# Kernel tuning notes

Measured on AMD Instinct MI355X. Metric: run time of the kernel, lower is better.

The kernel has to match this reference:

```python
import jax, jax.numpy as jnp
import numpy as np
import math

H = 128  # hidden_dim
RADIUS = 30.0


def _lin(x, w, b):
    return x @ w + b


def _masked_softmax(logits, mask):
    return jax.nn.softmax(jnp.where(mask, logits, -1e9), axis=-1)


def setup_inputs() -> dict:
    key = jax.random.key(0)
    ks = iter(jax.random.split(key, 64))

    def p(shape, s=0.02):
        return (jax.random.normal(next(ks), shape, jnp.float32) * s)

    B, N, T, M, L = 2, 48, 24, 192, 20
    inp = {
        'agents_state': jax.random.normal(next(ks), (B, N, T, 5), jnp.float32),
        'agents_mask': jnp.ones((B, N, T), jnp.float32),
        'map_polylines': jax.random.normal(next(ks), (B, M, L, 2), jnp.float32),
        'map_poly_mask': jnp.ones((B, M), jnp.float32),
        'map_poly_type': jax.random.randint(next(ks), (B, M), 0, 4),
        'map_tl_status': jax.random.randint(next(ks), (B, M), 0, 8),
        'map_on_route': jax.random.randint(next(ks), (B, M), 0, 2),
        # AgentStateEncoder
        'ae_w0': p((5, H)), 'ae_b0': p((H,)), 'ae_w1': p((H, H)), 'ae_b1': p((H,)),
        'ae_w2': p((H, H)), 'ae_b2': p((H,)),
        # MapPolylineNodeEncoder point_mlp
        'mp_w0': p((2, H)), 'mp_b0': p((H,)), 'mp_w1': p((H, H)), 'mp_b1': p((H,)),
        'type_emb': p((4, H)), 'tl_emb': p((8, H)), 'route_emb': p((2, H)),
        'mo_w0': p((H, H)), 'mo_b0': p((H,)), 'mo_w1': p((H, H)), 'mo_b1': p((H,)),
        # map_rel_mlp (3 -> H -> 1)
        'mr_w0': p((3, H)), 'mr_b0': p((H,)), 'mr_w1': p((H, 1)), 'mr_b1': p((1,)),
        # nbr_rel_mlp (5 -> H -> 1)
        'nr_w0': p((5, H)), 'nr_b0': p((H,)), 'nr_w1': p((H, 1)), 'nr_b1': p((1,)),
        # tau_out (3H -> H -> 64)
        'to_w0': p((3 * H, H)), 'to_b0': p((H,)), 'to_w1': p((H, 64)), 'to_b1': p((64,)),
    }
    return inp


def reference(agents_state, agents_mask, map_polylines, map_poly_mask,
              map_poly_type, map_tl_status, map_on_route,
              ae_w0, ae_b0, ae_w1, ae_b1, ae_w2, ae_b2,
              mp_w0, mp_b0, mp_w1, mp_b1, type_emb, tl_emb, route_emb,
              mo_w0, mo_b0, mo_w1, mo_b1,
              mr_w0, mr_b0, mr_w1, mr_b1,
              nr_w0, nr_b0, nr_w1, nr_b1,
              to_w0, to_b0, to_w1, to_b1):
    B, N, T, _ = agents_state.shape
    a_mask = agents_mask > 0.5
    a_feat = agents_state[..., :5]

    # --- MapPolylineNodeEncoder ---
    m = map_poly_mask > 0.5
    h = jax.nn.relu(_lin(jax.nn.relu(_lin(map_polylines, mp_w0, mp_b0)), mp_w1, mp_b1))  # B,M,L,H
    h = h.max(axis=2)  # B,M,H
    pt = jnp.clip(map_poly_type, 0, type_emb.shape[0] - 1)
    tl = jnp.clip(map_tl_status, 0, tl_emb.shape[0] - 1)
    rt = jnp.clip(map_on_route, 0, route_emb.shape[0] - 1)
    h = h + type_emb[pt] + tl_emb[tl] + route_emb[rt]
    h = _lin(jax.nn.relu(_lin(h, mo_w0, mo_b0)), mo_w1, mo_b1)
    map_node = h * m[..., None].astype(h.dtype)  # B,M,D
    map_center = map_polylines.mean(axis=2)  # B,M,2

    # --- AgentStateEncoder ---
    a = jax.nn.relu(_lin(a_feat, ae_w0, ae_b0))
    a = jax.nn.relu(_lin(a, ae_w1, ae_b1))
    a_emb = _lin(a, ae_w2, ae_b2) * a_mask[..., None].astype(a.dtype)  # B,N,T,D

    # --- map cross-attention with relative-position bias ---
    agent_pos = a_feat[..., 0:2]
    rel = map_center[:, None, None, :, :] - agent_pos[:, :, :, None, :]  # B,N,T,M,2
    dist = jnp.linalg.norm(rel, axis=-1, keepdims=True)
    rel_feat = jnp.concatenate([rel, dist], axis=-1)  # B,N,T,M,3
    rel_score = _lin(jax.nn.relu(_lin(rel_feat, mr_w0, mr_b0)), mr_w1, mr_b1)[..., 0]  # B,N,T,M
    dot = jnp.einsum('bntd,bmd->bntm', a_emb, map_node) / math.sqrt(map_node.shape[-1])
    attn = _masked_softmax(dot + rel_score, m[:, None, None, :])
    map_ctx = jnp.einsum('bntm,bmd->bntd', attn, map_node)

    # --- neighbor graph attention ---
    pos = a_feat[..., 0:2]
    vel = a_feat[..., 3:5]
    rel_pos = jnp.transpose(pos[:, :, None] - pos[:, None, :], (0, 1, 3, 2, 4))  # B,N,T,N,2
    rel_vel = jnp.transpose(vel[:, :, None] - vel[:, None, :], (0, 1, 3, 2, 4))
    dist_ij = jnp.linalg.norm(rel_pos, axis=-1, keepdims=True)  # B,N,T,N,1
    rel_ij = jnp.concatenate([rel_pos, rel_vel, dist_ij], axis=-1)  # B,N,T,N,5
    nbr_score = _lin(jax.nn.relu(_lin(rel_ij, nr_w0, nr_b0)), nr_w1, nr_b1)[..., 0]  # B,N,T,N

    valid_i = a_mask[..., None]  # B,N,T,1
    valid_j = jnp.transpose(a_mask, (0, 2, 1))[:, None, :, :]  # B,1,T,N
    radius_ok = dist_ij[..., 0] <= RADIUS
    not_self = ~jnp.eye(N, dtype=bool)[None, :, None, :]  # 1,N,1,N
    nbr_mask = valid_i & valid_j & radius_ok & not_self

    dot_n = jnp.einsum('bntd,bjtd->bntj', a_emb, a_emb) / math.sqrt(a_emb.shape[-1])
    w_n = _masked_softmax(dot_n + nbr_score, nbr_mask)  # B,N,T,N
    nbr_ctx = jnp.einsum('bntj,bjtd->bntd', w_n, a_emb)

    tau = jnp.concatenate([a_emb, map_ctx, nbr_ctx], axis=-1)
    tau = _lin(jax.nn.relu(_lin(tau, to_w0, to_b0)), to_w1, to_b1)
    tau = tau * a_mask[..., None].astype(tau.dtype)
    return tau, map_ctx, nbr_ctx
```

## Files before the change

kernel.cpp:

```cpp
#include <hip/hip_runtime.h>
#include <math.h>

#define HH 128
#define BB 2
#define NN 48
#define TT 24
#define MM 192
#define LL 20
#define NT (BB*NN*TT)
#define RSQRT_H 0.08838834764831845f
#define RADIUS_C 30.0f

struct P {
    const float *astate, *amask, *polylines, *poly_mask;
    const int *ptype, *tlst, *route;
    const float *ae_w0,*ae_b0,*ae_w1,*ae_b1,*ae_w2,*ae_b2;
    const float *mp_w0,*mp_b0,*mp_w1,*mp_b1;
    const float *type_emb,*tl_emb,*route_emb;
    const float *mo_w0,*mo_b0,*mo_w1,*mo_b1;
    const float *mr_w0,*mr_b0,*mr_w1,*mr_b1;
    const float *nr_w0,*nr_b0,*nr_w1,*nr_b1;
    const float *to_w0,*to_b0,*to_w1,*to_b1;
    float *tau,*map_ctx,*nbr_ctx;
    float *a_emb,*map_node,*map_nodeT,*map_center;
};

struct SME { float pts[LL*2]; float h1[LL][HH]; float mx[2][HH]; float hb[HH]; float pr[2][HH]; float hb2[HH]; };
struct SAG { float xin[4][5]; float h1[4][HH]; float h2[4][HH]; float p1[2][4][HH]; };
struct SMA { float mnL[16][MM]; float4 w4L[HH]; float w1L[HH]; float4 aq4L[HH]; float lg[4][MM]; float4 p4L[MM]; float invL[4]; float pc[2][4][HH]; };
struct SNB { float aVL[NN][129]; float pjL[NN][8]; float4 wAL[HH]; float4 wBL[HH]; float aqL[HH][8]; float sPL[4][6][NN]; float dPL[4][6][NN]; float lgL[6][NN]; float pL[NN][8]; float pcL[2][6][HH]; };
struct STA { float xinT[3*HH][4]; float p1L[2][4][HH]; float h1T[HH][4]; };

__device__ void do_map_enc(const P& p, SME& s, int bm) {
    int tid = threadIdx.x, pp = tid >> 7, c = tid & 127;
    if (tid < LL*2) s.pts[tid] = p.polylines[(size_t)bm*LL*2 + tid];
    __syncthreads();
    {
        float w0x = p.mp_w0[c], w0y = p.mp_w0[HH + c], b0 = p.mp_b0[c];
        #pragma unroll
        for (int i = 0; i < 10; ++i) {
            int pt_ = pp + 2*i;
            s.h1[pt_][c] = fmaxf(fmaf(s.pts[2*pt_], w0x, fmaf(s.pts[2*pt_+1], w0y, b0)), 0.f);
        }
    }
    if (tid < 2) {
        float sum = 0.f;
        for (int q = 0; q < LL; ++q) sum += s.pts[2*q + tid];
        p.map_center[bm*2 + tid] = sum * (1.0f / LL);
    }
    __syncthreads();
    {
        float acc[10];
        float b1 = p.mp_b1[c];
        #pragma unroll
        for (int i = 0; i < 10; ++i) acc[i] = b1;
        for (int k = 0; k < HH; ++k) {
            float wv = p.mp_w1[k*HH + c];
            #pragma unroll
            for (int i = 0; i < 10; ++i) acc[i] = fmaf(s.h1[pp + 2*i][k], wv, acc[i]);
        }
        float m10 = acc[0];
        #pragma unroll
        for (int i = 1; i < 10; ++i) m10 = fmaxf(m10, acc[i]);
        s.mx[pp][c] = m10;
    }
    __syncthreads();
    if (tid < HH) {
        float hm = fmaxf(fmaxf(s.mx[0][c], s.mx[1][c]), 0.f);
        int pt = p.ptype[bm]; pt = pt < 0 ? 0 : (pt > 3 ? 3 : pt);
        int tv = p.tlst[bm];  tv = tv < 0 ? 0 : (tv > 7 ? 7 : tv);
        int rv = p.route[bm]; rv = rv < 0 ? 0 : (rv > 1 ? 1 : rv);
        hm += p.type_emb[pt*HH + c] + p.tl_emb[tv*HH + c] + p.route_emb[rv*HH + c];
        s.hb[c] = hm;
    }
    __syncthreads();
    {
        float sum = 0.f;
        int k0 = pp*64;
        for (int k = k0; k < k0 + 64; ++k) sum = fmaf(s.hb[k], p.mo_w0[k*HH + c], sum);
        s.pr[pp][c] = sum;
    }
    __syncthreads();
    if (tid < HH) s.hb2[c] = fmaxf(s.pr[0][c] + s.pr[1][c] + p.mo_b0[c], 0.f);
    __syncthreads();
    {
        float sum = 0.f;
        int k0 = pp*64;
        for (int k = k0; k < k0 + 64; ++k) sum = fmaf(s.hb2[k], p.mo_w1[k*HH + c], sum);
        s.pr[pp][c] = sum;
    }
    __syncthreads();
    if (tid < HH) {
        float a3 = s.pr[0][c] + s.pr[1][c] + p.mo_b1[c];
        float mk = (p.poly_mask[bm] > 0.5f) ? 1.f : 0.f;
        float v = a3 * mk;
        p.map_node[(size_t)bm*HH + c] = v;
        int b = bm / MM, m = bm % MM;
        p.map_nodeT[((size_t)b*HH + c)*MM + m] = v;
    }
}

__device__ void do_agent_enc(const P& p, SAG& s, int r0) {
    int tid = threadIdx.x, h = tid >> 7, c = tid & 127;
    if (tid < 20) s.xin[tid/5][tid%5] = p.astate[(size_t)r0*5 + tid];
    __syncthreads();
    if (h == 0) {
        float b = p.ae_b0[c];
        float w[5];
        #pragma unroll
        for (int i = 0; i < 5; ++i) w[i] = p.ae_w0[i*HH + c];
        #pragma unroll
        for (int r = 0; r < 4; ++r) {
            float v = b;
            #pragma unroll
            for (int i = 0; i < 5; ++i) v = fmaf(s.xin[r][i], w[i], v);
            s.h1[r][c] = fmaxf(v, 0.f);
        }
    }
    __syncthreads();
    {
        float acc[4] = {0.f,0.f,0.f,0.f};
        int k0 = h*64;
        for (int k = k0; k < k0 + 64; ++k) {
            float wv = p.ae_w1[k*HH + c];
            #pragma unroll
            for (int r = 0; r < 4; ++r) acc[r] = fmaf(s.h1[r][k], wv, acc[r]);
        }
        #pragma unroll
        for (int r = 0; r < 4; ++r) s.p1[h][r][c] = acc[r];
    }
    __syncthreads();
    {
        #pragma unroll
        for (int rr = 0; rr < 2; ++rr) {
            int r = h*2 + rr;
            s.h2[r][c] = fmaxf(s.p1[0][r][c] + s.p1[1][r][c] + p.ae_b1[c], 0.f);
        }
    }
    __syncthreads();
    {
        float acc[4] = {0.f,0.f,0.f,0.f};
        int k0 = h*64;
        for (int k = k0; k < k0 + 64; ++k) {
            float wv = p.ae_w2[k*HH + c];
            #pragma unroll
            for (int r = 0; r < 4; ++r) acc[r] = fmaf(s.h2[r][k], wv, acc[r]);
        }
        #pragma unroll
        for (int r = 0; r < 4; ++r) s.p1[h][r][c] = acc[r];
    }
    __syncthreads();
    {
        #pragma unroll
        for (int rr = 0; rr < 2; ++rr) {
            int r = h*2 + rr;
            int row = r0 + r;
            p.a_emb[(size_t)row*HH + c] = (s.p1[0][r][c] + s.p1[1][r][c] + p.ae_b2[c]) * p.amask[row];
        }
    }
}

__device__ void do_map_attn(const P& p, SMA& s, int bnt0) {
    int b   = bnt0 / (NN*TT);
    int tid = threadIdx.x;

    if (tid < HH) {
        int k = tid;
        s.w4L[k] = make_float4(p.mr_w0[k], p.mr_w0[HH+k], p.mr_w0[2*HH+k], p.mr_b0[k]);
        s.w1L[k] = p.mr_w1[k];
    }
    for (int idx = tid; idx < 4*HH; idx += 256) {
        int r = idx >> 7, k = idx & 127;
        ((float*)&s.aq4L[k])[r] = p.a_emb[(size_t)(bnt0 + r)*HH + k];
    }

    float rx[4], ry[4], rd[4];
    if (tid < MM) {
        float mcx = p.map_center[(b*MM + tid)*2];
        float mcy = p.map_center[(b*MM + tid)*2 + 1];
        #pragma unroll
        for (int r = 0; r < 4; ++r) {
            float px = p.astate[(size_t)(bnt0 + r)*5];
            float py = p.astate[(size_t)(bnt0 + r)*5 + 1];
            rx[r] = mcx - px; ry[r] = mcy - py;
            rd[r] = sqrtf(rx[r]*rx[r] + ry[r]*ry[r]);
        }
    }

    const float* mnT = p.map_nodeT + (size_t)b*HH*MM;
    float4 st[3];
    #pragma unroll
    for (int i = 0; i < 3; ++i) {
        int q = tid + 256*i;
        int kk = q / 48, mq = q % 48;
        st[i] = *(const float4*)(mnT + (size_t)kk*MM + mq*4);
    }
    float sacc[4] = {0.f,0.f,0.f,0.f};
    float dt[4]   = {0.f,0.f,0.f,0.f};
    for (int ch = 0; ch < 8; ++ch) {
        __syncthreads();
        #pragma unroll
        for (int i = 0; i < 3; ++i) {
            int q = tid + 256*i;
            int kk = q / 48, mq = q % 48;
            *(float4*)&s.mnL[kk][mq*4] = st[i];
        }
        __syncthreads();
        if (ch < 7) {
            #pragma unroll
            for (int i = 0; i < 3; ++i) {
                int q = tid + 256*i;
                int kk = q / 48, mq = q % 48;
                st[i] = *(const float4*)(mnT + (size_t)(ch+1)*16*MM + (size_t)kk*MM + mq*4);
            }
        }
        if (tid < MM) {
            int k0 = ch*16;
            #pragma unroll
            for (int kk = 0; kk < 16; ++kk) {
                int k = k0 + kk;
                float4 w  = s.w4L[k];
                float  w1 = s.w1L[k];
                float4 aq = s.aq4L[k];
                float  mn = s.mnL[kk][tid];
                #pragma unroll
                for (int r = 0; r < 4; ++r) {
                    float hv = fmaf(rx[r], w.x, fmaf(ry[r], w.y, fmaf(rd[r], w.z, w.w)));
                    sacc[r] = fmaf(fmaxf(hv, 0.f), w1, sacc[r]);
                }
                dt[0] = fmaf(aq.x, mn, dt[0]);
                dt[1] = fmaf(aq.y, mn, dt[1]);
                dt[2] = fmaf(aq.z, mn, dt[2]);
                dt[3] = fmaf(aq.w, mn, dt[3]);
            }
        }
    }

    if (tid < MM) {
        float pm = p.poly_mask[b*MM + tid];
        float b1 = p.mr_b1[0];
        #pragma unroll
        for (int r = 0; r < 4; ++r) {
            float lgt = fmaf(dt[r], RSQRT_H, sacc[r] + b1);
            s.lg[r][tid] = (pm > 0.5f) ? lgt : -1e9f;
        }
    }
    __syncthreads();

    {
        int r = tid >> 6, l = tid & 63;
        float v = fmaxf(fmaxf(s.lg[r][l], s.lg[r][l+64]), s.lg[r][l+128]);
        #pragma unroll
        for (int o = 32; o > 0; o >>= 1) v = fmaxf(v, __shfl_xor(v, o));
        float e0 = expf(s.lg[r][l] - v);
        float e1 = expf(s.lg[r][l+64] - v);
        float e2 = expf(s.lg[r][l+128] - v);
        s.lg[r][l] = e0; s.lg[r][l+64] = e1; s.lg[r][l+128] = e2;
        float sm = e0 + e1 + e2;
        #pragma unroll
        for (int o = 32; o > 0; o >>= 1) sm += __shfl_xor(sm, o);
        if (l == 0) s.invL[r] = 1.0f / sm;
    }
    __syncthreads();
    if (tid < MM) {
        s.p4L[tid] = make_float4(s.lg[0][tid]*s.invL[0], s.lg[1][tid]*s.invL[1],
                                 s.lg[2][tid]*s.invL[2], s.lg[3][tid]*s.invL[3]);
    }
    __syncthreads();

    {
        int half = tid >> 7, c = tid & 127;
        float a0=0.f, a1=0.f, a2=0.f, a3=0.f;
        const float* mnb = p.map_node + ((size_t)b*MM + half*96)*HH + c;
        for (int m = 0; m < 96; ++m) {
            float mv = mnb[(size_t)m*HH];
            float4 pp4 = s.p4L[half*96 + m];
            a0 = fmaf(pp4.x, mv, a0); a1 = fmaf(pp4.y, mv, a1);
            a2 = fmaf(pp4.z, mv, a2); a3 = fmaf(pp4.w, mv, a3);
        }
        s.pc[half][0][c]=a0; s.pc[half][1][c]=a1; s.pc[half][2][c]=a2; s.pc[half][3][c]=a3;
    }
    __syncthreads();
    for (int idx = tid; idx < 4*HH; idx += 256) {
        int r = idx >> 7, c = idx & 127;
        p.map_ctx[(size_t)(bnt0 + r)*HH + c] = s.pc[0][r][c] + s.pc[1][r][c];
    }
}

__device__ void do_nbr_attn(const P& p, SNB& s, int task) {
    int b   = task / (TT*8);
    int rem = task % (TT*8);
    int t   = rem / 8;
    int n0  = (rem % 8) * 6;
    int tid = threadIdx.x;

    if (tid < NN) {
        int rj = (b*NN + tid)*TT + t;
        s.pjL[tid][0] = p.astate[(size_t)rj*5];
        s.pjL[tid][1] = p.astate[(size_t)rj*5 + 1];
        s.pjL[tid][2] = p.astate[(size_t)rj*5 + 3];
        s.pjL[tid][3] = p.astate[(size_t)rj*5 + 4];
        s.pjL[tid][4] = p.amask[rj];
    }
    if (tid < HH) {
        int k = tid;
        s.wAL[k] = make_float4(p.nr_w0[k], p.nr_w0[HH+k], p.nr_w0[2*HH+k], p.nr_w0[3*HH+k]);
        s.wBL[k] = make_float4(p.nr_w0[4*HH+k], p.nr_b0[k], p.nr_w1[k], 0.f);
    }
    #pragma unroll
    for (int i = 0; i < 6; ++i) {
        int q = tid + 256*i;
        int j = q >> 5, cq = q & 31;
        float4 v = *(const float4*)(p.a_emb + ((size_t)(b*NN + j)*TT + t)*HH + cq*4);
        s.aVL[j][cq*4+0] = v.x; s.aVL[j][cq*4+1] = v.y;
        s.aVL[j][cq*4+2] = v.z; s.aVL[j][cq*4+3] = v.w;
    }
    __syncthreads();
    for (int idx = tid; idx < 6*HH; idx += 256) {
        int r = idx >> 7, k = idx & 127;
        s.aqL[k][r] = s.aVL[n0 + r][k];
    }
    __syncthreads();

    {
        int j  = tid % 48;
        int kg = tid / 48;
        if (kg < 4) {
            float jx = s.pjL[j][0], jy = s.pjL[j][1], jvx = s.pjL[j][2], jvy = s.pjL[j][3];
            float dx[6], dy[6], dvx[6], dvy[6], dd[6];
            #pragma unroll
            for (int r = 0; r < 6; ++r) {
                dx[r]  = s.pjL[n0+r][0] - jx;  dy[r]  = s.pjL[n0+r][1] - jy;
                dvx[r] = s.pjL[n0+r][2] - jvx; dvy[r] = s.pjL[n0+r][3] - jvy;
                dd[r]  = sqrtf(dx[r]*dx[r] + dy[r]*dy[r]);
            }
            float sr[6]  = {0,0,0,0,0,0};
            float dt[6] = {0,0,0,0,0,0};
            int k0 = kg*32;
            for (int kk = 0; kk < 32; ++kk) {
                int k = k0 + kk;
                float4 wa = s.wAL[k], wb = s.wBL[k];
                float4 aA = *(const float4*)&s.aqL[k][0];
                float4 aB = *(const float4*)&s.aqL[k][4];
                float  av = s.aVL[j][k];
                #pragma unroll
                for (int r = 0; r < 6; ++r) {
                    float hv = fmaf(dx[r], wa.x, fmaf(dy[r], wa.y,
                               fmaf(dvx[r], wa.z, fmaf(dvy[r], wa.w,
                               fmaf(dd[r], wb.x, wb.y)))));
                    sr[r] = fmaf(fmaxf(hv, 0.f), wb.z, sr[r]);
                }
                dt[0] = fmaf(aA.x, av, dt[0]); dt[1] = fmaf(aA.y, av, dt[1]);
                dt[2] = fmaf(aA.z, av, dt[2]); dt[3] = fmaf(aA.w, av, dt[3]);
                dt[4] = fmaf(aB.x, av, dt[4]); dt[5] = fmaf(aB.y, av, dt[5]);
            }
            #pragma unroll
            for (int r = 0; r < 6; ++r) { s.sPL[kg][r][j] = sr[r]; s.dPL[kg][r][j] = dt[r]; }
        }
    }
    __syncthreads();

    float b1 = p.nr_b1[0];
    for (int idx = tid; idx < 6*NN; idx += 256) {
        int r = idx / NN, jj = idx % NN;
        int ni = n0 + r;
        float ss  = s.sPL[0][r][jj] + s.sPL[1][r][jj] + s.sPL[2][r][jj] + s.sPL[3][r][jj] + b1;
        float do2 = s.dPL[0][r][jj] + s.dPL[1][r][jj] + s.dPL[2][r][jj] + s.dPL[3][r][jj];
        float ddx = s.pjL[ni][0] - s.pjL[jj][0];
        float ddy = s.pjL[ni][1] - s.pjL[jj][1];
        float dist = sqrtf(ddx*ddx + ddy*ddy);
        bool ok = (s.pjL[ni][4] > 0.5f) && (s.pjL[jj][4] > 0.5f) &&
                  (dist <= RADIUS_C) && (jj != ni);
        s.lgL[r][jj] = ok ? fmaf(do2, RSQRT_H, ss) : -1e9f;
    }
    __syncthreads();

    {
        int wv = tid >> 6, l = tid & 63;
        for (int r = wv; r < 6; r += 4) {
            float v = (l < NN) ? s.lgL[r][l] : -3.4e38f;
            #pragma unroll
            for (int o = 32; o > 0; o >>= 1) v = fmaxf(v, __shfl_xor(v, o));
            float e = (l < NN) ? expf(s.lgL[r][l] - v) : 0.f;
            float sm = e;
            #pragma unroll
            for (int o = 32; o > 0; o >>= 1) sm += __shfl_xor(sm, o);
            if (l < NN) s.lgL[r][l] = e / sm;
        }
    }
    __syncthreads();
    if (tid < NN) {
        #pragma unroll
        for (int r = 0; r < 6; ++r) s.pL[tid][r] = s.lgL[r][tid];
        s.pL[tid][6] = 0.f; s.pL[tid][7] = 0.f;
    }
    __syncthreads();

    {
        int half = tid >> 7, c = tid & 127;
        float acc[6] = {0,0,0,0,0,0};
        for (int jj = half*24; jj < half*24 + 24; ++jj) {
            float av = s.aVL[jj][c];
            float4 pA = *(const float4*)&s.pL[jj][0];
            float4 pB = *(const float4*)&s.pL[jj][4];
            acc[0] = fmaf(pA.x, av, acc[0]); acc[1] = fmaf(pA.y, av, acc[1]);
            acc[2] = fmaf(pA.z, av, acc[2]); acc[3] = fmaf(pA.w, av, acc[3]);
            acc[4] = fmaf(pB.x, av, acc[4]); acc[5] = fmaf(pB.y, av, acc[5]);
        }
        #pragma unroll
        for (int r = 0; r < 6; ++r) s.pcL[half][r][c] = acc[r];
    }
    __syncthreads();
    for (int idx = tid; idx < 6*HH; idx += 256) {
        int r = idx >> 7, c = idx & 127;
        int row = (b*NN + n0 + r)*TT + t;
        p.nbr_ctx[(size_t)row*HH + c] = s.pcL[0][r][c] + s.pcL[1][r][c];
    }
}

__global__ __launch_bounds__(256) void k_enc(P p) {
    __shared__ __align__(16) char smraw[(sizeof(SME) > sizeof(SAG)) ? sizeof(SME) : sizeof(SAG)];
    int task = blockIdx.x;
    if (task < BB*MM) do_map_enc(p, *(SME*)smraw, task);
    else              do_agent_enc(p, *(SAG*)smraw, (task - BB*MM)*4);
}

__global__ __launch_bounds__(256) void k_attn(P p) {
    __shared__ __align__(16) char smraw[(sizeof(SMA) > sizeof(SNB)) ? sizeof(SMA) : sizeof(SNB)];
    int task = blockIdx.x;
    if (task < NT/4) do_map_attn(p, *(SMA*)smraw, task*4);
    else             do_nbr_attn(p, *(SNB*)smraw, task - NT/4);
}

__global__ __launch_bounds__(256) void k_tau(P p) {
    __shared__ __align__(16) STA s;
    int r0  = blockIdx.x * 4;
    int tid = threadIdx.x;
    for (int idx = tid; idx < 384; idx += 256) {
        int r = idx / 96, kq = idx % 96;
        const float* src; int co;
        if (kq < 32)      { src = p.a_emb;   co = kq; }
        else if (kq < 64) { src = p.map_ctx; co = kq - 32; }
        else              { src = p.nbr_ctx; co = kq - 64; }
        float4 v = *(const float4*)(src + (size_t)(r0 + r)*HH + co*4);
        int kb = (kq < 32 ? 0 : (kq < 64 ? HH : 2*HH)) + co*4;
        s.xinT[kb+0][r] = v.x; s.xinT[kb+1][r] = v.y;
        s.xinT[kb+2][r] = v.z; s.xinT[kb+3][r] = v.w;
    }
    __syncthreads();
    {
        int c = tid & 127, h = tid >> 7;
        float acc[4] = {0,0,0,0};
        for (int k = h*192; k < h*192 + 192; ++k) {
            float wv = p.to_w0[k*HH + c];
            float4 xa = *(const float4*)&s.xinT[k][0];
            acc[0]=fmaf(xa.x,wv,acc[0]); acc[1]=fmaf(xa.y,wv,acc[1]);
            acc[2]=fmaf(xa.z,wv,acc[2]); acc[3]=fmaf(xa.w,wv,acc[3]);
        }
        #pragma unroll
        for (int r = 0; r < 4; ++r) s.p1L[h][r][c] = acc[r];
    }
    __syncthreads();
    for (int idx = tid; idx < 4*HH; idx += 256) {
        int r = idx >> 7, k = idx & 127;
        s.h1T[k][r] = fmaxf(s.p1L[0][r][k] + s.p1L[1][r][k] + p.to_b0[k], 0.f);
    }
    __syncthreads();
    {
        int r = tid >> 6, c2 = tid & 63;
        float acc = p.to_b1[c2];
        for (int k = 0; k < HH; ++k)
            acc = fmaf(s.h1T[k][r], p.to_w1[k*64 + c2], acc);
        p.tau[(size_t)(r0 + r)*64 + c2] = acc * p.amask[r0 + r];
    }
}

extern "C" void kernel_launch(void* const* d_in, const int* in_sizes, int n_in,
                              void* d_out, int out_size, void* d_ws, size_t ws_size,
                              hipStream_t stream)
{
    P p;
    p.astate    = (const float*)d_in[0];
    p.amask     = (const float*)d_in[1];
    p.polylines = (const float*)d_in[2];
    p.poly_mask = (const float*)d_in[3];
    p.ptype     = (const int*)d_in[4];
    p.tlst      = (const int*)d_in[5];
    p.route     = (const int*)d_in[6];
    p.ae_w0 = (const float*)d_in[7];  p.ae_b0 = (const float*)d_in[8];
    p.ae_w1 = (const float*)d_in[9];  p.ae_b1 = (const float*)d_in[10];
    p.ae_w2 = (const float*)d_in[11]; p.ae_b2 = (const float*)d_in[12];
    p.mp_w0 = (const float*)d_in[13]; p.mp_b0 = (const float*)d_in[14];
    p.mp_w1 = (const float*)d_in[15]; p.mp_b1 = (const float*)d_in[16];
    p.type_emb  = (const float*)d_in[17];
    p.tl_emb    = (const float*)d_in[18];
    p.route_emb = (const float*)d_in[19];
    p.mo_w0 = (const float*)d_in[20]; p.mo_b0 = (const float*)d_in[21];
    p.mo_w1 = (const float*)d_in[22]; p.mo_b1 = (const float*)d_in[23];
    p.mr_w0 = (const float*)d_in[24]; p.mr_b0 = (const float*)d_in[25];
    p.mr_w1 = (const float*)d_in[26]; p.mr_b1 = (const float*)d_in[27];
    p.nr_w0 = (const float*)d_in[28]; p.nr_b0 = (const float*)d_in[29];
    p.nr_w1 = (const float*)d_in[30]; p.nr_b1 = (const float*)d_in[31];
    p.to_w0 = (const float*)d_in[32]; p.to_b0 = (const float*)d_in[33];
    p.to_w1 = (const float*)d_in[34]; p.to_b1 = (const float*)d_in[35];

    p.tau     = (float*)d_out;
    p.map_ctx = (float*)d_out + (size_t)NT*64;
    p.nbr_ctx = p.map_ctx + (size_t)NT*HH;

    float* ws    = (float*)d_ws;
    p.a_emb      = ws;
    p.map_node   = p.a_emb + (size_t)NT*HH;
    p.map_nodeT  = p.map_node + (size_t)BB*MM*HH;
    p.map_center = p.map_nodeT + (size_t)BB*MM*HH;

    k_enc <<<BB*MM + NT/4,        256, 0, stream>>>(p);
    k_attn<<<NT/4 + BB*TT*8,      256, 0, stream>>>(p);
    k_tau <<<NT/4,                256, 0, stream>>>(p);
}
```

Measured before the change: 184.4 us.

## Prefetch weights and intermediates into cache and halve rows per tau block

Each kernel now opens with a distributed float4 touch of the weights or intermediate buffers it will read (MLP weights in k_enc, a_emb/map_node/map_nodeT in k_attn, tau weights in k_tau), pinned by an empty asm so the loads are not removed. The aim is to warm the L2 cache before the compute phases need the data. k_tau also processes 2 rows per block instead of 4, doubling the grid, and splits the second layer's K reduction across both thread halves. This adds redundant memory traffic and repeated weight reads across more blocks in exchange for more parallelism and warmer caches.

New measurement: 189.3 us. 2.6% more time.

```diff
diff --git a/kernel.cpp b/kernel.cpp
--- a/kernel.cpp
+++ b/kernel.cpp
@@ -25,11 +25,15 @@
     float *a_emb,*map_node,*map_nodeT,*map_center;
 };
 
+__device__ __forceinline__ void keep4(float4 v) {
+    asm volatile("" :: "v"(v.x), "v"(v.y), "v"(v.z), "v"(v.w));
+}
+
 struct SME { float pts[LL*2]; float h1[LL][HH]; float mx[2][HH]; float hb[HH]; float pr[2][HH]; float hb2[HH]; };
 struct SAG { float xin[4][5]; float h1[4][HH]; float h2[4][HH]; float p1[2][4][HH]; };
 struct SMA { float mnL[16][MM]; float4 w4L[HH]; float w1L[HH]; float4 aq4L[HH]; float lg[4][MM]; float4 p4L[MM]; float invL[4]; float pc[2][4][HH]; };
 struct SNB { float aVL[NN][129]; float pjL[NN][8]; float4 wAL[HH]; float4 wBL[HH]; float aqL[HH][8]; float sPL[4][6][NN]; float dPL[4][6][NN]; float lgL[6][NN]; float pL[NN][8]; float pcL[2][6][HH]; };
-struct STA { float xinT[3*HH][4]; float p1L[2][4][HH]; float h1T[HH][4]; };
+struct STA2 { float xinT[3*HH][2]; float p1L[2][2][HH]; float h1T[HH][2]; };
 
 __device__ void do_map_enc(const P& p, SME& s, int bm) {
     int tid = threadIdx.x, pp = tid >> 7, c = tid & 127;
@@ -419,6 +423,17 @@
 }
 
 __global__ __launch_bounds__(256) void k_enc(P p) {
+    {
+        int sgl = (blockIdx.x % 80) * 256 + threadIdx.x;
+        int mi  = sgl >> 12;
+        int off = (sgl & 4095) << 2;
+        const float* base = p.mp_w1;
+        if (mi == 1) base = p.mo_w0;
+        else if (mi == 2) base = p.mo_w1;
+        else if (mi == 3) base = p.ae_w1;
+        else if (mi == 4) base = p.ae_w2;
+        keep4(*(const float4*)(base + off));
+    }
     __shared__ __align__(16) char smraw[(sizeof(SME) > sizeof(SAG)) ? sizeof(SME) : sizeof(SAG)];
     int task = blockIdx.x;
     if (task < BB*MM) do_map_enc(p, *(SME*)smraw, task);
@@ -426,6 +441,16 @@
 }
 
 __global__ __launch_bounds__(256) void k_attn(P p) {
+    {
+        int g = blockIdx.x * 256 + threadIdx.x;
+        if (g < 98304) {
+            const float* base; int off;
+            if (g < 73728)      { base = p.a_emb;     off = g * 4; }
+            else if (g < 86016) { base = p.map_node;  off = (g - 73728) * 4; }
+            else                { base = p.map_nodeT; off = (g - 86016) * 4; }
+            keep4(*(const float4*)(base + off));
+        }
+    }
     __shared__ __align__(16) char smraw[(sizeof(SMA) > sizeof(SNB)) ? sizeof(SMA) : sizeof(SNB)];
     int task = blockIdx.x;
     if (task < NT/4) do_map_attn(p, *(SMA*)smraw, task*4);
@@ -433,11 +458,21 @@
 }
 
 __global__ __launch_bounds__(256) void k_tau(P p) {
-    __shared__ __align__(16) STA s;
-    int r0  = blockIdx.x * 4;
+    {
+        int g = blockIdx.x * 256 + threadIdx.x;
+        if (g < 14336) {
+            const float* base; int off;
+            if (g < 12288) { base = p.to_w0; off = g * 4; }
+            else           { base = p.to_w1; off = (g - 12288) * 4; }
+            keep4(*(const float4*)(base + off));
+        }
+    }
+    __shared__ __align__(16) STA2 s;
+    int r0  = blockIdx.x * 2;
     int tid = threadIdx.x;
-    for (int idx = tid; idx < 384; idx += 256) {
-        int r = idx / 96, kq = idx % 96;
+
+    if (tid < 192) {
+        int r = tid / 96, kq = tid % 96;
         const float* src; int co;
         if (kq < 32)      { src = p.a_emb;   co = kq; }
         else if (kq < 64) { src = p.map_ctx; co = kq - 32; }
@@ -450,28 +485,35 @@
     __syncthreads();
     {
         int c = tid & 127, h = tid >> 7;
-        float acc[4] = {0,0,0,0};
+        float a0 = 0.f, a1 = 0.f;
         for (int k = h*192; k < h*192 + 192; ++k) {
             float wv = p.to_w0[k*HH + c];
-            float4 xa = *(const float4*)&s.xinT[k][0];
-            acc[0]=fmaf(xa.x,wv,acc[0]); acc[1]=fmaf(xa.y,wv,acc[1]);
-            acc[2]=fmaf(xa.z,wv,acc[2]); acc[3]=fmaf(xa.w,wv,acc[3]);
-        }
-        #pragma unroll
-        for (int r = 0; r < 4; ++r) s.p1L[h][r][c] = acc[r];
-    }
-    __syncthreads();
-    for (int idx = tid; idx < 4*HH; idx += 256) {
-        int r = idx >> 7, k = idx & 127;
+            float2 x = *(const float2*)&s.xinT[k][0];
+            a0 = fmaf(x.x, wv, a0);
+            a1 = fmaf(x.y, wv, a1);
+        }
+        s.p1L[h][0][c] = a0;
+        s.p1L[h][1][c] = a1;
+    }
+    __syncthreads();
+    {
+        int r = tid >> 7, k = tid & 127;
         s.h1T[k][r] = fmaxf(s.p1L[0][r][k] + s.p1L[1][r][k] + p.to_b0[k], 0.f);
     }
     __syncthreads();
     {
+        int kh = tid >> 7, rc = tid & 127;
+        int r = rc >> 6, c2 = rc & 63;
+        float acc = 0.f;
+        for (int k = kh*64; k < kh*64 + 64; ++k)
+            acc = fmaf(s.h1T[k][r], p.to_w1[k*64 + c2], acc);
+        s.p1L[kh][r][c2] = acc;
+    }
+    __syncthreads();
+    if (tid < 128) {
         int r = tid >> 6, c2 = tid & 63;
-        float acc = p.to_b1[c2];
-        for (int k = 0; k < HH; ++k)
-            acc = fmaf(s.h1T[k][r], p.to_w1[k*64 + c2], acc);
-        p.tau[(size_t)(r0 + r)*64 + c2] = acc * p.amask[r0 + r];
+        float v = (s.p1L[0][r][c2] + s.p1L[1][r][c2] + p.to_b1[c2]) * p.amask[r0 + r];
+        p.tau[(size_t)(r0 + r)*64 + c2] = v;
     }
 }
 
@@ -514,7 +556,7 @@
     p.map_nodeT  = p.map_node + (size_t)BB*MM*HH;
     p.map_center = p.map_nodeT + (size_t)BB*MM*HH;
 
-    k_enc <<<BB*MM + NT/4,        256, 0, stream>>>(p);
-    k_attn<<<NT/4 + BB*TT*8,      256, 0, stream>>>(p);
-    k_tau <<<NT/4,                256, 0, stream>>>(p);
-}
+    k_enc <<<BB*MM + NT/4,   256, 0, stream>>>(p);
+    k_attn<<<NT/4 + BB*TT*8, 256, 0, stream>>>(p);
+    k_tau <<<NT/2,           256, 0, stream>>>(p);
+}
```

## Fuse map attention, neighbor attention and tau MLP into one kernel

Applied to the files above, without the earlier changes.

Replaces the separate attention and tau kernels with one fused kernel where each block handles 4 agents at one timestep. It computes map attention, neighbor attention and the tau MLP, keeping map_ctx and nbr_ctx in shared memory instead of rereading them from global memory. Shared memory is overlaid with a union across phases, and neighbor embeddings are read directly from global memory instead of being staged. This removes one launch and the tau input reloads, but each block now runs the three phases serially, so there are fewer blocks and less parallel overlap between map and neighbor work.

Result: no change. 187.9 us (+1.9%).

```diff
diff --git a/kernel.cpp b/kernel.cpp
--- a/kernel.cpp
+++ b/kernel.cpp
@@ -27,9 +27,36 @@
 
 struct SME { float pts[LL*2]; float h1[LL][HH]; float mx[2][HH]; float hb[HH]; float pr[2][HH]; float hb2[HH]; };
 struct SAG { float xin[4][5]; float h1[4][HH]; float h2[4][HH]; float p1[2][4][HH]; };
-struct SMA { float mnL[16][MM]; float4 w4L[HH]; float w1L[HH]; float4 aq4L[HH]; float lg[4][MM]; float4 p4L[MM]; float invL[4]; float pc[2][4][HH]; };
-struct SNB { float aVL[NN][129]; float pjL[NN][8]; float4 wAL[HH]; float4 wBL[HH]; float aqL[HH][8]; float sPL[4][6][NN]; float dPL[4][6][NN]; float lgL[6][NN]; float pL[NN][8]; float pcL[2][6][HH]; };
-struct STA { float xinT[3*HH][4]; float p1L[2][4][HH]; float h1T[HH][4]; };
+
+struct SF {
+    float4 aq4L[HH];
+    float  mctx[4][HH];
+    float  nctx[4][HH];
+    float  pc[2][4][HH];
+    union {
+        struct {
+            float  mnL[16][MM];
+            float4 w4L[HH];
+            float  w1L[HH];
+            float  lg[4][MM];
+            float4 p4L[MM];
+            float  invL[4];
+        } m;
+        struct {
+            float  pjL[NN][8];
+            float4 wAL[HH];
+            float4 wBL[HH];
+            float  sPL[4][4][NN];
+            float  dPL[4][4][NN];
+            float  lgN[4][NN];
+            float4 pN[NN];
+        } n;
+        struct {
+            float  xinT[3*HH][4];
+            float  h1T[HH][4];
+        } t;
+    } u;
+};
 
 __device__ void do_map_enc(const P& p, SME& s, int bm) {
     int tid = threadIdx.x, pp = tid >> 7, c = tid & 127;
@@ -160,18 +187,32 @@
     }
 }
 
-__device__ void do_map_attn(const P& p, SMA& s, int bnt0) {
-    int b   = bnt0 / (NN*TT);
-    int tid = threadIdx.x;
-
+__global__ __launch_bounds__(256) void k_enc(P p) {
+    __shared__ __align__(16) char smraw[(sizeof(SME) > sizeof(SAG)) ? sizeof(SME) : sizeof(SAG)];
+    int task = blockIdx.x;
+    if (task < BB*MM) do_map_enc(p, *(SME*)smraw, task);
+    else              do_agent_enc(p, *(SAG*)smraw, (task - BB*MM)*4);
+}
+
+__global__ __launch_bounds__(256) void k_fat(P p) {
+    __shared__ __align__(16) SF s;
+    int task = blockIdx.x;
+    int b    = task / (TT*12);
+    int rem  = task % (TT*12);
+    int t    = rem / 12;
+    int n0   = (rem % 12) * 4;
+    int tid  = threadIdx.x;
+
+    int row0 = (b*NN + n0)*TT + t;
+
+    for (int idx = tid; idx < 4*HH; idx += 256) {
+        int r = idx >> 7, k = idx & 127;
+        ((float*)&s.aq4L[k])[r] = p.a_emb[(size_t)(row0 + r*TT)*HH + k];
+    }
     if (tid < HH) {
         int k = tid;
-        s.w4L[k] = make_float4(p.mr_w0[k], p.mr_w0[HH+k], p.mr_w0[2*HH+k], p.mr_b0[k]);
-        s.w1L[k] = p.mr_w1[k];
-    }
-    for (int idx = tid; idx < 4*HH; idx += 256) {
-        int r = idx >> 7, k = idx & 127;
-        ((float*)&s.aq4L[k])[r] = p.a_emb[(size_t)(bnt0 + r)*HH + k];
+        s.u.m.w4L[k] = make_float4(p.mr_w0[k], p.mr_w0[HH+k], p.mr_w0[2*HH+k], p.mr_b0[k]);
+        s.u.m.w1L[k] = p.mr_w1[k];
     }
 
     float rx[4], ry[4], rd[4];
@@ -180,8 +221,8 @@
         float mcy = p.map_center[(b*MM + tid)*2 + 1];
         #pragma unroll
         for (int r = 0; r < 4; ++r) {
-            float px = p.astate[(size_t)(bnt0 + r)*5];
-            float py = p.astate[(size_t)(bnt0 + r)*5 + 1];
+            float px = p.astate[(size_t)(row0 + r*TT)*5];
+            float py = p.astate[(size_t)(row0 + r*TT)*5 + 1];
             rx[r] = mcx - px; ry[r] = mcy - py;
             rd[r] = sqrtf(rx[r]*rx[r] + ry[r]*ry[r]);
         }
@@ -196,14 +237,14 @@
         st[i] = *(const float4*)(mnT + (size_t)kk*MM + mq*4);
     }
     float sacc[4] = {0.f,0.f,0.f,0.f};
-    float dt[4]   = {0.f,0.f,0.f,0.f};
+    float dt4[4]  = {0.f,0.f,0.f,0.f};
     for (int ch = 0; ch < 8; ++ch) {
         __syncthreads();
         #pragma unroll
         for (int i = 0; i < 3; ++i) {
             int q = tid + 256*i;
             int kk = q / 48, mq = q % 48;
-            *(float4*)&s.mnL[kk][mq*4] = st[i];
+            *(float4*)&s.u.m.mnL[kk][mq*4] = st[i];
         }
         __syncthreads();
         if (ch < 7) {
@@ -219,52 +260,51 @@
             #pragma unroll
             for (int kk = 0; kk < 16; ++kk) {
                 int k = k0 + kk;
-                float4 w  = s.w4L[k];
-                float  w1 = s.w1L[k];
+                float4 w  = s.u.m.w4L[k];
+                float  w1 = s.u.m.w1L[k];
                 float4 aq = s.aq4L[k];
-                float  mn = s.mnL[kk][tid];
+                float  mn = s.u.m.mnL[kk][tid];
                 #pragma unroll
                 for (int r = 0; r < 4; ++r) {
                     float hv = fmaf(rx[r], w.x, fmaf(ry[r], w.y, fmaf(rd[r], w.z, w.w)));
                     sacc[r] = fmaf(fmaxf(hv, 0.f), w1, sacc[r]);
                 }
-                dt[0] = fmaf(aq.x, mn, dt[0]);
-                dt[1] = fmaf(aq.y, mn, dt[1]);
-                dt[2] = fmaf(aq.z, mn, dt[2]);
-                dt[3] = fmaf(aq.w, mn, dt[3]);
+                dt4[0] = fmaf(aq.x, mn, dt4[0]);
+                dt4[1] = fmaf(aq.y, mn, dt4[1]);
+                dt4[2] = fmaf(aq.z, mn, dt4[2]);
+                dt4[3] = fmaf(aq.w, mn, dt4[3]);
             }
         }
     }
-
     if (tid < MM) {
         float pm = p.poly_mask[b*MM + tid];
         float b1 = p.mr_b1[0];
         #pragma unroll
         for (int r = 0; r < 4; ++r) {
-            float lgt = fmaf(dt[r], RSQRT_H, sacc[r] + b1);
-            s.lg[r][tid] = (pm > 0.5f) ? lgt : -1e9f;
+            float lgt = fmaf(dt4[r], RSQRT_H, sacc[r] + b1);
+            s.u.m.lg[r][tid] = (pm > 0.5f) ? lgt : -1e9f;
         }
     }
     __syncthreads();
 
     {
         int r = tid >> 6, l = tid & 63;
-        float v = fmaxf(fmaxf(s.lg[r][l], s.lg[r][l+64]), s.lg[r][l+128]);
+        float v = fmaxf(fmaxf(s.u.m.lg[r][l], s.u.m.lg[r][l+64]), s.u.m.lg[r][l+128]);
         #pragma unroll
         for (int o = 32; o > 0; o >>= 1) v = fmaxf(v, __shfl_xor(v, o));
-        float e0 = expf(s.lg[r][l] - v);
-        float e1 = expf(s.lg[r][l+64] - v);
-        float e2 = expf(s.lg[r][l+128] - v);
-        s.lg[r][l] = e0; s.lg[r][l+64] = e1; s.lg[r][l+128] = e2;
+        float e0 = expf(s.u.m.lg[r][l] - v);
+        float e1 = expf(s.u.m.lg[r][l+64] - v);
+        float e2 = expf(s.u.m.lg[r][l+128] - v);
+        s.u.m.lg[r][l] = e0; s.u.m.lg[r][l+64] = e1; s.u.m.lg[r][l+128] = e2;
         float sm = e0 + e1 + e2;
         #pragma unroll
         for (int o = 32; o > 0; o >>= 1) sm += __shfl_xor(sm, o);
-        if (l == 0) s.invL[r] = 1.0f / sm;
+        if (l == 0) s.u.m.invL[r] = 1.0f / sm;
     }
     __syncthreads();
     if (tid < MM) {
-        s.p4L[tid] = make_float4(s.lg[0][tid]*s.invL[0], s.lg[1][tid]*s.invL[1],
-                                 s.lg[2][tid]*s.invL[2], s.lg[3][tid]*s.invL[3]);
+        s.u.m.p4L[tid] = make_float4(s.u.m.lg[0][tid]*s.u.m.invL[0], s.u.m.lg[1][tid]*s.u.m.invL[1],
+                                     s.u.m.lg[2][tid]*s.u.m.invL[2], s.u.m.lg[3][tid]*s.u.m.invL[3]);
     }
     __syncthreads();
 
@@ -274,7 +314,7 @@
         const float* mnb = p.map_node + ((size_t)b*MM + half*96)*HH + c;
         for (int m = 0; m < 96; ++m) {
             float mv = mnb[(size_t)m*HH];
-            float4 pp4 = s.p4L[half*96 + m];
+            float4 pp4 = s.u.m.p4L[half*96 + m];
             a0 = fmaf(pp4.x, mv, a0); a1 = fmaf(pp4.y, mv, a1);
             a2 = fmaf(pp4.z, mv, a2); a3 = fmaf(pp4.w, mv, a3);
         }
@@ -283,42 +323,24 @@
     __syncthreads();
     for (int idx = tid; idx < 4*HH; idx += 256) {
         int r = idx >> 7, c = idx & 127;
-        p.map_ctx[(size_t)(bnt0 + r)*HH + c] = s.pc[0][r][c] + s.pc[1][r][c];
-    }
-}
-
-__device__ void do_nbr_attn(const P& p, SNB& s, int task) {
-    int b   = task / (TT*8);
-    int rem = task % (TT*8);
-    int t   = rem / 8;
-    int n0  = (rem % 8) * 6;
-    int tid = threadIdx.x;
+        float v = s.pc[0][r][c] + s.pc[1][r][c];
+        s.mctx[r][c] = v;
+        p.map_ctx[(size_t)(row0 + r*TT)*HH + c] = v;
+    }
+    __syncthreads();
 
     if (tid < NN) {
         int rj = (b*NN + tid)*TT + t;
-        s.pjL[tid][0] = p.astate[(size_t)rj*5];
-        s.pjL[tid][1] = p.astate[(size_t)rj*5 + 1];
-        s.pjL[tid][2] = p.astate[(size_t)rj*5 + 3];
-        s.pjL[tid][3] = p.astate[(size_t)rj*5 + 4];
-        s.pjL[tid][4] = p.amask[rj];
+        s.u.n.pjL[tid][0] = p.astate[(size_t)rj*5];
+        s.u.n.pjL[tid][1] = p.astate[(size_t)rj*5 + 1];
+        s.u.n.pjL[tid][2] = p.astate[(size_t)rj*5 + 3];
+        s.u.n.pjL[tid][3] = p.astate[(size_t)rj*5 + 4];
+        s.u.n.pjL[tid][4] = p.amask[rj];
     }
     if (tid < HH) {
         int k = tid;
-        s.wAL[k] = make_float4(p.nr_w0[k], p.nr_w0[HH+k], p.nr_w0[2*HH+k], p.nr_w0[3*HH+k]);
-        s.wBL[k] = make_float4(p.nr_w0[4*HH+k], p.nr_b0[k], p.nr_w1[k], 0.f);
-    }
-    #pragma unroll
-    for (int i = 0; i < 6; ++i) {
-        int q = tid + 256*i;
-        int j = q >> 5, cq = q & 31;
-        float4 v = *(const float4*)(p.a_emb + ((size_t)(b*NN + j)*TT + t)*HH + cq*4);
-        s.aVL[j][cq*4+0] = v.x; s.aVL[j][cq*4+1] = v.y;
-        s.aVL[j][cq*4+2] = v.z; s.aVL[j][cq*4+3] = v.w;
-    }
-    __syncthreads();
-    for (int idx = tid; idx < 6*HH; idx += 256) {
-        int r = idx >> 7, k = idx & 127;
-        s.aqL[k][r] = s.aVL[n0 + r][k];
+        s.u.n.wAL[k] = make_float4(p.nr_w0[k], p.nr_w0[HH+k], p.nr_w0[2*HH+k], p.nr_w0[3*HH+k]);
+        s.u.n.wBL[k] = make_float4(p.nr_w0[4*HH+k], p.nr_b0[k], p.nr_w1[k], 0.f);
     }
     __syncthreads();
 
@@ -326,126 +348,101 @@
         int j  = tid % 48;
         int kg = tid / 48;
         if (kg < 4) {
-            float jx = s.pjL[j][0], jy = s.pjL[j][1], jvx = s.pjL[j][2], jvy = s.pjL[j][3];
-            float dx[6], dy[6], dvx[6], dvy[6], dd[6];
-            #pragma unroll
-            for (int r = 0; r < 6; ++r) {
-                dx[r]  = s.pjL[n0+r][0] - jx;  dy[r]  = s.pjL[n0+r][1] - jy;
-                dvx[r] = s.pjL[n0+r][2] - jvx; dvy[r] = s.pjL[n0+r][3] - jvy;
+            float jx = s.u.n.pjL[j][0], jy = s.u.n.pjL[j][1];
+            float jvx = s.u.n.pjL[j][2], jvy = s.u.n.pjL[j][3];
+            float dx[4], dy[4], dvx[4], dvy[4], dd[4];
+            #pragma unroll
+            for (int r = 0; r < 4; ++r) {
+                int ni = n0 + r;
+                dx[r]  = s.u.n.pjL[ni][0] - jx;  dy[r]  = s.u.n.pjL[ni][1] - jy;
+                dvx[r] = s.u.n.pjL[ni][2] - jvx; dvy[r] = s.u.n.pjL[ni][3] - jvy;
                 dd[r]  = sqrtf(dx[r]*dx[r] + dy[r]*dy[r]);
             }
-            float sr[6]  = {0,0,0,0,0,0};
-            float dt[6] = {0,0,0,0,0,0};
+            const float* aj = p.a_emb + ((size_t)(b*NN + j)*TT + t)*HH;
+            float sr[4]  = {0,0,0,0};
+            float dtn[4] = {0,0,0,0};
             int k0 = kg*32;
             for (int kk = 0; kk < 32; ++kk) {
                 int k = k0 + kk;
-                float4 wa = s.wAL[k], wb = s.wBL[k];
-                float4 aA = *(const float4*)&s.aqL[k][0];
-                float4 aB = *(const float4*)&s.aqL[k][4];
-                float  av = s.aVL[j][k];
+                float4 wa = s.u.n.wAL[k], wb = s.u.n.wBL[k];
+                float4 aq = s.aq4L[k];
+                float  av = aj[k];
                 #pragma unroll
-                for (int r = 0; r < 6; ++r) {
+                for (int r = 0; r < 4; ++r) {
                     float hv = fmaf(dx[r], wa.x, fmaf(dy[r], wa.y,
                                fmaf(dvx[r], wa.z, fmaf(dvy[r], wa.w,
                                fmaf(dd[r], wb.x, wb.y)))));
                     sr[r] = fmaf(fmaxf(hv, 0.f), wb.z, sr[r]);
                 }
-                dt[0] = fmaf(aA.x, av, dt[0]); dt[1] = fmaf(aA.y, av, dt[1]);
-                dt[2] = fmaf(aA.z, av, dt[2]); dt[3] = fmaf(aA.w, av, dt[3]);
-                dt[4] = fmaf(aB.x, av, dt[4]); dt[5] = fmaf(aB.y, av, dt[5]);
+                dtn[0] = fmaf(aq.x, av, dtn[0]); dtn[1] = fmaf(aq.y, av, dtn[1]);
+                dtn[2] = fmaf(aq.z, av, dtn[2]); dtn[3] = fmaf(aq.w, av, dtn[3]);
             }
             #pragma unroll
-            for (int r = 0; r < 6; ++r) { s.sPL[kg][r][j] = sr[r]; s.dPL[kg][r][j] = dt[r]; }
-        }
-    }
-    __syncthreads();
-
-    float b1 = p.nr_b1[0];
-    for (int idx = tid; idx < 6*NN; idx += 256) {
-        int r = idx / NN, jj = idx % NN;
-        int ni = n0 + r;
-        float ss  = s.sPL[0][r][jj] + s.sPL[1][r][jj] + s.sPL[2][r][jj] + s.sPL[3][r][jj] + b1;
-        float do2 = s.dPL[0][r][jj] + s.dPL[1][r][jj] + s.dPL[2][r][jj] + s.dPL[3][r][jj];
-        float ddx = s.pjL[ni][0] - s.pjL[jj][0];
-        float ddy = s.pjL[ni][1] - s.pjL[jj][1];
-        float dist = sqrtf(ddx*ddx + ddy*ddy);
-        bool ok = (s.pjL[ni][4] > 0.5f) && (s.pjL[jj][4] > 0.5f) &&
-                  (dist <= RADIUS_C) && (jj != ni);
-        s.lgL[r][jj] = ok ? fmaf(do2, RSQRT_H, ss) : -1e9f;
-    }
-    __syncthreads();
-
-    {
-        int wv = tid >> 6, l = tid & 63;
-        for (int r = wv; r < 6; r += 4) {
-            float v = (l < NN) ? s.lgL[r][l] : -3.4e38f;
-            #pragma unroll
-            for (int o = 32; o > 0; o >>= 1) v = fmaxf(v, __shfl_xor(v, o));
-            float e = (l < NN) ? expf(s.lgL[r][l] - v) : 0.f;
-            float sm = e;
-            #pragma unroll
-            for (int o = 32; o > 0; o >>= 1) sm += __shfl_xor(sm, o);
-            if (l < NN) s.lgL[r][l] = e / sm;
-        }
+            for (int r = 0; r < 4; ++r) { s.u.n.sPL[kg][r][j] = sr[r]; s.u.n.dPL[kg][r][j] = dtn[r]; }
+        }
+    }
+    __syncthreads();
+
+    {
+        float b1 = p.nr_b1[0];
+        for (int idx = tid; idx < 4*NN; idx += 256) {
+            int r = idx / NN, jj = idx % NN;
+            int ni = n0 + r;
+            float ss  = s.u.n.sPL[0][r][jj] + s.u.n.sPL[1][r][jj] + s.u.n.sPL[2][r][jj] + s.u.n.sPL[3][r][jj] + b1;
+            float do2 = s.u.n.dPL[0][r][jj] + s.u.n.dPL[1][r][jj] + s.u.n.dPL[2][r][jj] + s.u.n.dPL[3][r][jj];
+            float ddx = s.u.n.pjL[ni][0] - s.u.n.pjL[jj][0];
+            float ddy = s.u.n.pjL[ni][1] - s.u.n.pjL[jj][1];
+            float dist = sqrtf(ddx*ddx + ddy*ddy);
+            bool ok = (s.u.n.pjL[ni][4] > 0.5f) && (s.u.n.pjL[jj][4] > 0.5f) &&
+                      (dist <= RADIUS_C) && (jj != ni);
+            s.u.n.lgN[r][jj] = ok ? fmaf(do2, RSQRT_H, ss) : -1e9f;
+        }
+    }
+    __syncthreads();
+
+    {
+        int r = tid >> 6, l = tid & 63;
+        float v = (l < NN) ? s.u.n.lgN[r][l] : -3.4e38f;
+        #pragma unroll
+        for (int o = 32; o > 0; o >>= 1) v = fmaxf(v, __shfl_xor(v, o));
+        float e = (l < NN) ? expf(s.u.n.lgN[r][l] - v) : 0.f;
+        float sm = e;
+        #pragma unroll
+        for (int o = 32; o > 0; o >>= 1) sm += __shfl_xor(sm, o);
+        if (l < NN) s.u.n.lgN[r][l] = e / sm;
     }
     __syncthreads();
     if (tid < NN) {
-        #pragma unroll
-        for (int r = 0; r < 6; ++r) s.pL[tid][r] = s.lgL[r][tid];
-        s.pL[tid][6] = 0.f; s.pL[tid][7] = 0.f;
+        s.u.n.pN[tid] = make_float4(s.u.n.lgN[0][tid], s.u.n.lgN[1][tid],
+                                    s.u.n.lgN[2][tid], s.u.n.lgN[3][tid]);
     }
     __syncthreads();
 
     {
         int half = tid >> 7, c = tid & 127;
-        float acc[6] = {0,0,0,0,0,0};
+        float a0=0.f, a1=0.f, a2=0.f, a3=0.f;
         for (int jj = half*24; jj < half*24 + 24; ++jj) {
-            float av = s.aVL[jj][c];
-            float4 pA = *(const float4*)&s.pL[jj][0];
-            float4 pB = *(const float4*)&s.pL[jj][4];
-            acc[0] = fmaf(pA.x, av, acc[0]); acc[1] = fmaf(pA.y, av, acc[1]);
-            acc[2] = fmaf(pA.z, av, acc[2]); acc[3] = fmaf(pA.w, av, acc[3]);
-            acc[4] = fmaf(pB.x, av, acc[4]); acc[5] = fmaf(pB.y, av, acc[5]);
-        }
-        #pragma unroll
-        for (int r = 0; r < 6; ++r) s.pcL[half][r][c] = acc[r];
-    }
-    __syncthreads();
-    for (int idx = tid; idx < 6*HH; idx += 256) {
+            float av = p.a_emb[((size_t)(b*NN + jj)*TT + t)*HH + c];
+            float4 pp4 = s.u.n.pN[jj];
+            a0 = fmaf(pp4.x, av, a0); a1 = fmaf(pp4.y, av, a1);
+            a2 = fmaf(pp4.z, av, a2); a3 = fmaf(pp4.w, av, a3);
+        }
+        s.pc[half][0][c]=a0; s.pc[half][1][c]=a1; s.pc[half][2][c]=a2; s.pc[half][3][c]=a3;
+    }
+    __syncthreads();
+    for (int idx = tid; idx < 4*HH; idx += 256) {
         int r = idx >> 7, c = idx & 127;
-        int row = (b*NN + n0 + r)*TT + t;
-        p.nbr_ctx[(size_t)row*HH + c] = s.pcL[0][r][c] + s.pcL[1][r][c];
-    }
-}
-
-__global__ __launch_bounds__(256) void k_enc(P p) {
-    __shared__ __align__(16) char smraw[(sizeof(SME) > sizeof(SAG)) ? sizeof(SME) : sizeof(SAG)];
-    int task = blockIdx.x;
-    if (task < BB*MM) do_map_enc(p, *(SME*)smraw, task);
-    else              do_agent_enc(p, *(SAG*)smraw, (task - BB*MM)*4);
-}
-
-__global__ __launch_bounds__(256) void k_attn(P p) {
-    __shared__ __align__(16) char smraw[(sizeof(SMA) > sizeof(SNB)) ? sizeof(SMA) : sizeof(SNB)];
-    int task = blockIdx.x;
-    if (task < NT/4) do_map_attn(p, *(SMA*)smraw, task*4);
-    else             do_nbr_attn(p, *(SNB*)smraw, task - NT/4);
-}
-
-__global__ __launch_bounds__(256) void k_tau(P p) {
-    __shared__ __align__(16) STA s;
-    int r0  = blockIdx.x * 4;
-    int tid = threadIdx.x;
-    for (int idx = tid; idx < 384; idx += 256) {
-        int r = idx / 96, kq = idx % 96;
-        const float* src; int co;
-        if (kq < 32)      { src = p.a_emb;   co = kq; }
-        else if (kq < 64) { src = p.map_ctx; co = kq - 32; }
-        else              { src = p.nbr_ctx; co = kq - 64; }
-        float4 v = *(const float4*)(src + (size_t)(r0 + r)*HH + co*4);
-        int kb = (kq < 32 ? 0 : (kq < 64 ? HH : 2*HH)) + co*4;
-        s.xinT[kb+0][r] = v.x; s.xinT[kb+1][r] = v.y;
-        s.xinT[kb+2][r] = v.z; s.xinT[kb+3][r] = v.w;
+        float v = s.pc[0][r][c] + s.pc[1][r][c];
+        s.nctx[r][c] = v;
+        p.nbr_ctx[(size_t)(row0 + r*TT)*HH + c] = v;
+    }
+    __syncthreads();
+
+    for (int idx = tid; idx < 4*HH; idx += 256) {
+        int r = idx >> 7, k = idx & 127;
+        s.u.t.xinT[k][r]        = ((float*)&s.aq4L[k])[r];
+        s.u.t.xinT[HH + k][r]   = s.mctx[r][k];
+        s.u.t.xinT[2*HH + k][r] = s.nctx[r][k];
     }
     __syncthreads();
     {
@@ -453,25 +450,25 @@
         float acc[4] = {0,0,0,0};
         for (int k = h*192; k < h*192 + 192; ++k) {
             float wv = p.to_w0[k*HH + c];
-            float4 xa = *(const float4*)&s.xinT[k][0];
+            float4 xa = *(const float4*)&s.u.t.xinT[k][0];
             acc[0]=fmaf(xa.x,wv,acc[0]); acc[1]=fmaf(xa.y,wv,acc[1]);
             acc[2]=fmaf(xa.z,wv,acc[2]); acc[3]=fmaf(xa.w,wv,acc[3]);
         }
         #pragma unroll
-        for (int r = 0; r < 4; ++r) s.p1L[h][r][c] = acc[r];
+        for (int r = 0; r < 4; ++r) s.pc[h][r][c] = acc[r];
     }
     __syncthreads();
     for (int idx = tid; idx < 4*HH; idx += 256) {
         int r = idx >> 7, k = idx & 127;
-        s.h1T[k][r] = fmaxf(s.p1L[0][r][k] + s.p1L[1][r][k] + p.to_b0[k], 0.f);
+        s.u.t.h1T[k][r] = fmaxf(s.pc[0][r][k] + s.pc[1][r][k] + p.to_b0[k], 0.f);
     }
     __syncthreads();
     {
         int r = tid >> 6, c2 = tid & 63;
         float acc = p.to_b1[c2];
         for (int k = 0; k < HH; ++k)
-            acc = fmaf(s.h1T[k][r], p.to_w1[k*64 + c2], acc);
-        p.tau[(size_t)(r0 + r)*64 + c2] = acc * p.amask[r0 + r];
+            acc = fmaf(s.u.t.h1T[k][r], p.to_w1[k*64 + c2], acc);
+        p.tau[(size_t)(row0 + r*TT)*64 + c2] = acc * p.amask[row0 + r*TT];
     }
 }
 
@@ -514,7 +511,6 @@
     p.map_nodeT  = p.map_node + (size_t)BB*MM*HH;
     p.map_center = p.map_nodeT + (size_t)BB*MM*HH;
 
-    k_enc <<<BB*MM + NT/4,        256, 0, stream>>>(p);
-    k_attn<<<NT/4 + BB*TT*8,      256, 0, stream>>>(p);
-    k_tau <<<NT/4,                256, 0, stream>>>(p);
+    k_enc<<<BB*MM + NT/4, 256, 0, stream>>>(p);
+    k_fat<<<BB*TT*12,     256, 0, stream>>>(p);
 }
```
